# Kernel tuning notes

Hardware: AMD Instinct MI355X
Metric: run time of the kernel (lower is better)

The kernel has to match this reference:

```python
import jax, jax.numpy as jnp
import numpy as np

NHID = 1024
# Canonical DARTS recurrent genotype: (activation, predecessor-state index)
GENOTYPE = [("sigmoid", 0), ("relu", 1), ("relu", 1), ("identity", 1),
            ("tanh", 2), ("sigmoid", 5), ("tanh", 3), ("relu", 5)]
CONCAT = [1, 2, 3, 4, 5, 6, 7, 8]

_ACTS = {"tanh": jnp.tanh, "relu": jax.nn.relu,
         "sigmoid": jax.nn.sigmoid, "identity": lambda z: z}


def _cell(x, h_prev, W0, Ws):
    # x: [B, ninp], h_prev: [B, nhid]
    xh = jnp.concatenate([x, h_prev], axis=-1)              # [B, ninp+nhid]
    c0, h0 = jnp.split(xh @ W0, 2, axis=-1)                 # each [B, nhid]
    s0 = h_prev + jax.nn.sigmoid(c0) * (jnp.tanh(h0) - h_prev)
    states = [s0]
    for i, (name, pred) in enumerate(GENOTYPE):
        s_prev = states[pred]
        c, h = jnp.split(s_prev @ Ws[i], 2, axis=-1)
        s = s_prev + jax.nn.sigmoid(c) * (_ACTS[name](h) - s_prev)
        states.append(s)
    return jnp.mean(jnp.stack([states[i] for i in CONCAT], axis=-1), axis=-1)


def setup_inputs() -> dict:
    key = jax.random.key(0)
    k1, k2, k3 = jax.random.split(key, 3)
    T, B, NINP = 256, 256, 1024
    inputs = jax.random.normal(k1, (T, B, NINP), dtype=jnp.float32)
    h0 = jnp.zeros((B, NHID), dtype=jnp.float32)
    W0 = jax.random.normal(k2, (NINP + NHID, 2 * NHID), dtype=jnp.float32) * 0.02
    Ws = jax.random.normal(k3, (len(GENOTYPE), NHID, 2 * NHID), dtype=jnp.float32) * 0.02
    return {"inputs": inputs, "h0": h0, "W0": W0, "Ws": Ws}


def reference(inputs, h0, W0, Ws):
    def step(h, x):
        h_new = _cell(x, h, W0, Ws)
        return h_new, h_new
    _, hiddens = jax.lax.scan(step, h0, inputs)             # [T, B, nhid]
    return hiddens
```

## Files before the change

### kernel.cpp

```cpp
#include <hip/hip_runtime.h>


typedef short short8 __attribute__((ext_vector_type(8)));
typedef float floatx4 __attribute__((ext_vector_type(4)));

__device__ __forceinline__ unsigned short f2bf(float f) {
  unsigned u = __builtin_bit_cast(unsigned, f);
  u += 0x7fffu + ((u >> 16) & 1u);
  return (unsigned short)(u >> 16);
}

enum { ACT_SIG = 0, ACT_RELU = 1, ACT_TANH = 2, ACT_ID = 3 };

__device__ __forceinline__ float actf(int a, float h) {
  if (a == ACT_SIG)  return 1.f / (1.f + __expf(-h));
  if (a == ACT_RELU) return fmaxf(h, 0.f);
  if (a == ACT_TANH) return 1.f - 2.f / (__expf(2.f * h) + 1.f);
  return h;
}

struct Job {
  const float* A;
  const float* A2;
  const unsigned short* Wt;
  const float* base;
  float* out;
  int act;
  int pad;
};
struct Jobs3 { Job j[3]; };

__global__ __launch_bounds__(256) void cell_gemm(Jobs3 jobs, int K) {
  const Job jb = jobs.j[blockIdx.z];
  const int j0c = blockIdx.x * 32;
  const int m0  = blockIdx.y * 64;

  __shared__ __align__(16) unsigned short As[64][40];
  __shared__ __align__(16) unsigned short Bs[64][40];

  const int tid  = threadIdx.x;
  const int r    = tid >> 2;
  const int kq   = (tid & 3) * 8;
  const int lane = tid & 63;
  const int wave = tid >> 6;
  const int col  = lane & 15;
  const int quad = lane >> 4;

  floatx4 acc[4];
#pragma unroll
  for (int i = 0; i < 4; ++i) acc[i] = (floatx4){0.f, 0.f, 0.f, 0.f};

  const int n_glob = (r < 32) ? (j0c + r) : (1024 + j0c + (r - 32));
  const unsigned short* wrow = jb.Wt + (size_t)n_glob * K;

  for (int k0 = 0; k0 < K; k0 += 32) {
    const float* Ap; int kk;
    if (jb.A2 != nullptr && k0 >= 1024) { Ap = jb.A2; kk = k0 - 1024; }
    else                                { Ap = jb.A;  kk = k0; }

    const float4* ap = reinterpret_cast<const float4*>(Ap + (size_t)(m0 + r) * 1024 + kk + kq);
    float4 f0 = ap[0];
    float4 f1 = ap[1];
    uint4 packed;
    packed.x = (unsigned)f2bf(f0.x) | ((unsigned)f2bf(f0.y) << 16);
    packed.y = (unsigned)f2bf(f0.z) | ((unsigned)f2bf(f0.w) << 16);
    packed.z = (unsigned)f2bf(f1.x) | ((unsigned)f2bf(f1.y) << 16);
    packed.w = (unsigned)f2bf(f1.z) | ((unsigned)f2bf(f1.w) << 16);
    *reinterpret_cast<uint4*>(&As[r][kq]) = packed;

    *reinterpret_cast<uint4*>(&Bs[r][kq]) =
        *reinterpret_cast<const uint4*>(wrow + k0 + kq);

    __syncthreads();

    short8 a = *reinterpret_cast<const short8*>(&As[wave * 16 + col][quad * 8]);
#pragma unroll
    for (int nt = 0; nt < 4; ++nt) {
      short8 b = *reinterpret_cast<const short8*>(&Bs[nt * 16 + col][quad * 8]);
      acc[nt] = __builtin_amdgcn_mfma_f32_16x16x32_bf16(a, b, acc[nt], 0, 0, 0);
    }
    __syncthreads();
  }

#pragma unroll
  for (int nt = 0; nt < 2; ++nt) {
#pragma unroll
    for (int rr = 0; rr < 4; ++rr) {
      int m = m0 + wave * 16 + quad * 4 + rr;
      int n = j0c + nt * 16 + col;
      float c = acc[nt][rr];
      float h = acc[nt + 2][rr];
      float p = jb.base[(size_t)m * 1024 + n];
      float g = 1.f / (1.f + __expf(-c));
      float av = actf(jb.act, h);
      jb.out[(size_t)m * 1024 + n] = fmaf(g, av - p, p);
    }
  }
}

__global__ __launch_bounds__(256) void conv_w(const float* __restrict__ W0,
                                              const float* __restrict__ Wsrc,
                                              unsigned short* __restrict__ wt) {
  int job = blockIdx.z;
  int K = (job == 0) ? 2048 : 1024;
  int kt = blockIdx.y;
  if (kt * 32 >= K) return;
  int nt = blockIdx.x;
  const float* W = (job == 0) ? W0 : (Wsrc + (size_t)(job - 1) * 1024 * 2048);
  unsigned short* Wt = (job == 0) ? wt
      : (wt + (size_t)2048 * 2048 + (size_t)(job - 1) * 2048 * 1024);

  __shared__ unsigned short tile[32][33];
  int tx = threadIdx.x & 31;
  int ty = threadIdx.x >> 5;
#pragma unroll
  for (int i = 0; i < 4; ++i) {
    int k = kt * 32 + ty + i * 8;
    tile[ty + i * 8][tx] = f2bf(W[(size_t)k * 2048 + nt * 32 + tx]);
  }
  __syncthreads();
#pragma unroll
  for (int i = 0; i < 4; ++i) {
    int n = nt * 32 + ty + i * 8;
    Wt[(size_t)n * K + kt * 32 + tx] = tile[tx][ty + i * 8];
  }
}

__global__ __launch_bounds__(256) void mean8(
    const float* __restrict__ s1, const float* __restrict__ s2,
    const float* __restrict__ s3, const float* __restrict__ s4,
    const float* __restrict__ s5, const float* __restrict__ s6,
    const float* __restrict__ s7, const float* __restrict__ s8,
    float* __restrict__ out) {
  int i = blockIdx.x * 256 + threadIdx.x;
  float4 v1 = reinterpret_cast<const float4*>(s1)[i];
  float4 v2 = reinterpret_cast<const float4*>(s2)[i];
  float4 v3 = reinterpret_cast<const float4*>(s3)[i];
  float4 v4 = reinterpret_cast<const float4*>(s4)[i];
  float4 v5 = reinterpret_cast<const float4*>(s5)[i];
  float4 v6 = reinterpret_cast<const float4*>(s6)[i];
  float4 v7 = reinterpret_cast<const float4*>(s7)[i];
  float4 v8 = reinterpret_cast<const float4*>(s8)[i];
  float4 o;
  o.x = (v1.x + v2.x + v3.x + v4.x + v5.x + v6.x + v7.x + v8.x) * 0.125f;
  o.y = (v1.y + v2.y + v3.y + v4.y + v5.y + v6.y + v7.y + v8.y) * 0.125f;
  o.z = (v1.z + v2.z + v3.z + v4.z + v5.z + v6.z + v7.z + v8.z) * 0.125f;
  o.w = (v1.w + v2.w + v3.w + v4.w + v5.w + v6.w + v7.w + v8.w) * 0.125f;
  reinterpret_cast<float4*>(out)[i] = o;
}

extern "C" void kernel_launch(void* const* d_in, const int* in_sizes, int n_in,
                              void* d_out, int out_size, void* d_ws, size_t ws_size,
                              hipStream_t stream) {
  const float* x_all = (const float*)d_in[0];
  const float* h0    = (const float*)d_in[1];
  const float* W0    = (const float*)d_in[2];
  const float* Ws    = (const float*)d_in[3];
  float* out = (float*)d_out;

  unsigned short* wt0 = (unsigned short*)d_ws;
  unsigned short* wts[8];
  for (int i = 0; i < 8; ++i)
    wts[i] = wt0 + (size_t)2048 * 2048 + (size_t)i * 2048 * 1024;
  float* sbuf = (float*)((char*)d_ws + (size_t)(2048 * 2048 + 8 * 2048 * 1024) * 2);
  float* s[9];
  for (int i = 0; i < 9; ++i) s[i] = sbuf + (size_t)i * 256 * 1024;

  conv_w<<<dim3(64, 64, 9), 256, 0, stream>>>(W0, Ws, wt0);

  const size_t BH = (size_t)256 * 1024;
  for (int t = 0; t < 256; ++t) {
    const float* x_t = x_all + (size_t)t * BH;
    const float* hp  = (t == 0) ? h0 : (out + (size_t)(t - 1) * BH);
    float* o_t = out + (size_t)t * BH;

    Jobs3 J{};
    J.j[0] = { x_t, hp, wt0, hp, s[0], ACT_TANH, 0 };
    cell_gemm<<<dim3(32, 4, 1), 256, 0, stream>>>(J, 2048);

    J = Jobs3{};
    J.j[0] = { s[0], nullptr, wts[0], s[0], s[1], ACT_SIG, 0 };
    cell_gemm<<<dim3(32, 4, 1), 256, 0, stream>>>(J, 1024);

    J = Jobs3{};
    J.j[0] = { s[1], nullptr, wts[1], s[1], s[2], ACT_RELU, 0 };
    J.j[1] = { s[1], nullptr, wts[2], s[1], s[3], ACT_RELU, 0 };
    J.j[2] = { s[1], nullptr, wts[3], s[1], s[4], ACT_ID,   0 };
    cell_gemm<<<dim3(32, 4, 3), 256, 0, stream>>>(J, 1024);

    J = Jobs3{};
    J.j[0] = { s[2], nullptr, wts[4], s[2], s[5], ACT_TANH, 0 };
    J.j[1] = { s[3], nullptr, wts[6], s[3], s[7], ACT_TANH, 0 };
    cell_gemm<<<dim3(32, 4, 2), 256, 0, stream>>>(J, 1024);

    J = Jobs3{};
    J.j[0] = { s[5], nullptr, wts[5], s[5], s[6], ACT_SIG,  0 };
    J.j[1] = { s[5], nullptr, wts[7], s[5], s[8], ACT_RELU, 0 };
    cell_gemm<<<dim3(32, 4, 2), 256, 0, stream>>>(J, 1024);

    mean8<<<dim3(256), 256, 0, stream>>>(s[1], s[2], s[3], s[4],
                                         s[5], s[6], s[7], s[8], o_t);
  }
}
```

Measured before the change: 46.12 ms.

## Keep states in bf16, drop LDS staging, fuse final phase with mean and next-input prep

Each stage now writes a bf16 copy of its output, so the next GEMM reads bf16 operands directly instead of converting fp32 activations on every load. The GEMM drops shared-memory tiling for direct register loads with double-buffered MFMA on larger 64x64 per-block tiles. Launches are rebalanced: the identity branch moves to the third phase, and the last two GEMMs, the 8-way mean, and packing of the next x_t/h into a bf16 buffer are fused into one kernel. This removes the separate mean kernel and repeated fp32→bf16 conversion, at the cost of fewer blocks per launch (64 vs 128) and uncoalesced-ish direct global loads with no LDS reuse.

```diff
diff --git a/kernel.cpp b/kernel.cpp
--- a/kernel.cpp
+++ b/kernel.cpp
@@ -3,6 +3,10 @@
 
 typedef short short8 __attribute__((ext_vector_type(8)));
 typedef float floatx4 __attribute__((ext_vector_type(4)));
+
+#define MFMA __builtin_amdgcn_mfma_f32_16x16x32_bf16
+
+enum { ACT_SIG = 0, ACT_RELU = 1, ACT_TANH = 2, ACT_ID = 3 };
 
 __device__ __forceinline__ unsigned short f2bf(float f) {
   unsigned u = __builtin_bit_cast(unsigned, f);
@@ -10,92 +14,209 @@
   return (unsigned short)(u >> 16);
 }
 
-enum { ACT_SIG = 0, ACT_RELU = 1, ACT_TANH = 2, ACT_ID = 3 };
+__device__ __forceinline__ float sigf(float z) { return 1.f / (1.f + __expf(-z)); }
 
 __device__ __forceinline__ float actf(int a, float h) {
-  if (a == ACT_SIG)  return 1.f / (1.f + __expf(-h));
+  if (a == ACT_SIG)  return sigf(h);
   if (a == ACT_RELU) return fmaxf(h, 0.f);
   if (a == ACT_TANH) return 1.f - 2.f / (__expf(2.f * h) + 1.f);
   return h;
 }
 
-struct Job {
-  const float* A;
-  const float* A2;
+
+struct GJob {
+  const unsigned short* A;
   const unsigned short* Wt;
   const float* base;
-  float* out;
+  float* out_f;
+  unsigned short* out_b;
   int act;
-  int pad;
+  int K;
 };
-struct Jobs3 { Job j[3]; };
-
-__global__ __launch_bounds__(256) void cell_gemm(Jobs3 jobs, int K) {
-  const Job jb = jobs.j[blockIdx.z];
-  const int j0c = blockIdx.x * 32;
-  const int m0  = blockIdx.y * 64;
-
-  __shared__ __align__(16) unsigned short As[64][40];
-  __shared__ __align__(16) unsigned short Bs[64][40];
-
-  const int tid  = threadIdx.x;
-  const int r    = tid >> 2;
-  const int kq   = (tid & 3) * 8;
-  const int lane = tid & 63;
-  const int wave = tid >> 6;
-  const int col  = lane & 15;
-  const int quad = lane >> 4;
-
-  floatx4 acc[4];
-#pragma unroll
-  for (int i = 0; i < 4; ++i) acc[i] = (floatx4){0.f, 0.f, 0.f, 0.f};
-
-  const int n_glob = (r < 32) ? (j0c + r) : (1024 + j0c + (r - 32));
-  const unsigned short* wrow = jb.Wt + (size_t)n_glob * K;
-
-  for (int k0 = 0; k0 < K; k0 += 32) {
-    const float* Ap; int kk;
-    if (jb.A2 != nullptr && k0 >= 1024) { Ap = jb.A2; kk = k0 - 1024; }
-    else                                { Ap = jb.A;  kk = k0; }
-
-    const float4* ap = reinterpret_cast<const float4*>(Ap + (size_t)(m0 + r) * 1024 + kk + kq);
-    float4 f0 = ap[0];
-    float4 f1 = ap[1];
-    uint4 packed;
-    packed.x = (unsigned)f2bf(f0.x) | ((unsigned)f2bf(f0.y) << 16);
-    packed.y = (unsigned)f2bf(f0.z) | ((unsigned)f2bf(f0.w) << 16);
-    packed.z = (unsigned)f2bf(f1.x) | ((unsigned)f2bf(f1.y) << 16);
-    packed.w = (unsigned)f2bf(f1.z) | ((unsigned)f2bf(f1.w) << 16);
-    *reinterpret_cast<uint4*>(&As[r][kq]) = packed;
-
-    *reinterpret_cast<uint4*>(&Bs[r][kq]) =
-        *reinterpret_cast<const uint4*>(wrow + k0 + kq);
-
-    __syncthreads();
-
-    short8 a = *reinterpret_cast<const short8*>(&As[wave * 16 + col][quad * 8]);
-#pragma unroll
-    for (int nt = 0; nt < 4; ++nt) {
-      short8 b = *reinterpret_cast<const short8*>(&Bs[nt * 16 + col][quad * 8]);
-      acc[nt] = __builtin_amdgcn_mfma_f32_16x16x32_bf16(a, b, acc[nt], 0, 0, 0);
+struct GJobs { GJob j[3]; };
+
+struct Set6 { short8 a0, a1, b0, b1, b2, b3; };
+
+__device__ __forceinline__ void load6(Set6& s,
+    const unsigned short* pa0, const unsigned short* pa1,
+    const unsigned short* pb0, const unsigned short* pb1,
+    const unsigned short* pb2, const unsigned short* pb3, int k) {
+  s.a0 = *(const short8*)(pa0 + k);
+  s.a1 = *(const short8*)(pa1 + k);
+  s.b0 = *(const short8*)(pb0 + k);
+  s.b1 = *(const short8*)(pb1 + k);
+  s.b2 = *(const short8*)(pb2 + k);
+  s.b3 = *(const short8*)(pb3 + k);
+}
+
+__device__ __forceinline__ void mm6(const Set6& s, floatx4 ac[2][2], floatx4 ah[2][2]) {
+  ac[0][0] = MFMA(s.a0, s.b0, ac[0][0], 0, 0, 0);
+  ac[1][0] = MFMA(s.a1, s.b0, ac[1][0], 0, 0, 0);
+  ac[0][1] = MFMA(s.a0, s.b1, ac[0][1], 0, 0, 0);
+  ac[1][1] = MFMA(s.a1, s.b1, ac[1][1], 0, 0, 0);
+  ah[0][0] = MFMA(s.a0, s.b2, ah[0][0], 0, 0, 0);
+  ah[1][0] = MFMA(s.a1, s.b2, ah[1][0], 0, 0, 0);
+  ah[0][1] = MFMA(s.a0, s.b3, ah[0][1], 0, 0, 0);
+  ah[1][1] = MFMA(s.a1, s.b3, ah[1][1], 0, 0, 0);
+}
+
+__global__ __launch_bounds__(256) void phase_gemm(GJobs jobs) {
+  const GJob jb = jobs.j[blockIdx.z];
+  const int K = jb.K;
+  const int lane = threadIdx.x & 63;
+  const int wave = threadIdx.x >> 6;
+  const int col = lane & 15, quad = lane >> 4;
+  const int m0  = blockIdx.y * 64 + (wave >> 1) * 32;
+  const int sc0 = blockIdx.x * 64 + (wave & 1) * 32;
+
+  const unsigned short* pa0 = jb.A + (size_t)(m0 + col) * K + quad * 8;
+  const unsigned short* pa1 = pa0 + (size_t)16 * K;
+  const unsigned short* pb0 = jb.Wt + (size_t)(sc0 + col) * K + quad * 8;
+  const unsigned short* pb1 = pb0 + (size_t)16 * K;
+  const unsigned short* pb2 = jb.Wt + (size_t)(1024 + sc0 + col) * K + quad * 8;
+  const unsigned short* pb3 = pb2 + (size_t)16 * K;
+
+  floatx4 ac[2][2], ah[2][2];
+#pragma unroll
+  for (int i = 0; i < 2; ++i)
+#pragma unroll
+    for (int j = 0; j < 2; ++j) {
+      ac[i][j] = (floatx4){0.f, 0.f, 0.f, 0.f};
+      ah[i][j] = (floatx4){0.f, 0.f, 0.f, 0.f};
     }
-    __syncthreads();
-  }
-
-#pragma unroll
-  for (int nt = 0; nt < 2; ++nt) {
-#pragma unroll
-    for (int rr = 0; rr < 4; ++rr) {
-      int m = m0 + wave * 16 + quad * 4 + rr;
-      int n = j0c + nt * 16 + col;
-      float c = acc[nt][rr];
-      float h = acc[nt + 2][rr];
-      float p = jb.base[(size_t)m * 1024 + n];
-      float g = 1.f / (1.f + __expf(-c));
-      float av = actf(jb.act, h);
-      jb.out[(size_t)m * 1024 + n] = fmaf(g, av - p, p);
-    }
-  }
+
+  Set6 s0, s1;
+  load6(s0, pa0, pa1, pb0, pb1, pb2, pb3, 0);
+  load6(s1, pa0, pa1, pb0, pb1, pb2, pb3, 32);
+  for (int k = 64; k < K; k += 64) {
+    mm6(s0, ac, ah);
+    load6(s0, pa0, pa1, pb0, pb1, pb2, pb3, k);
+    mm6(s1, ac, ah);
+    load6(s1, pa0, pa1, pb0, pb1, pb2, pb3, k + 32);
+  }
+  mm6(s0, ac, ah);
+  mm6(s1, ac, ah);
+
+  const int act = jb.act;
+#pragma unroll
+  for (int mi = 0; mi < 2; ++mi)
+#pragma unroll
+    for (int ni = 0; ni < 2; ++ni)
+#pragma unroll
+      for (int rr = 0; rr < 4; ++rr) {
+        int m = m0 + mi * 16 + quad * 4 + rr;
+        int n = sc0 + ni * 16 + col;
+        int idx = m * 1024 + n;
+        float c = ac[mi][ni][rr];
+        float h = ah[mi][ni][rr];
+        float p = jb.base[idx];
+        float v = fmaf(sigf(c), actf(act, h) - p, p);
+        jb.out_f[idx] = v;
+        if (jb.out_b) jb.out_b[idx] = f2bf(v);
+      }
+}
+
+struct Set10 { short8 a0, a1, u0, u1, u2, u3, v0, v1, v2, v3; };
+
+__global__ __launch_bounds__(256) void phase_e(
+    const unsigned short* __restrict__ A,
+    const unsigned short* __restrict__ W5t,
+    const unsigned short* __restrict__ W7t,
+    const float* __restrict__ m1, const float* __restrict__ m2,
+    const float* __restrict__ m3, const float* __restrict__ m4,
+    const float* __restrict__ m5, const float* __restrict__ m7,
+    const float* __restrict__ xnext,
+    float* __restrict__ out_t,
+    unsigned short* __restrict__ xhb) {
+  const int lane = threadIdx.x & 63;
+  const int wave = threadIdx.x >> 6;
+  const int col = lane & 15, quad = lane >> 4;
+  const int m0  = blockIdx.y * 64 + (wave >> 1) * 32;
+  const int sc0 = blockIdx.x * 64 + (wave & 1) * 32;
+  const int K = 1024;
+
+  const unsigned short* pa0 = A + (size_t)(m0 + col) * K + quad * 8;
+  const unsigned short* pa1 = pa0 + (size_t)16 * K;
+  const unsigned short* pu0 = W5t + (size_t)(sc0 + col) * K + quad * 8;
+  const unsigned short* pu1 = pu0 + (size_t)16 * K;
+  const unsigned short* pu2 = W5t + (size_t)(1024 + sc0 + col) * K + quad * 8;
+  const unsigned short* pu3 = pu2 + (size_t)16 * K;
+  const unsigned short* pv0 = W7t + (size_t)(sc0 + col) * K + quad * 8;
+  const unsigned short* pv1 = pv0 + (size_t)16 * K;
+  const unsigned short* pv2 = W7t + (size_t)(1024 + sc0 + col) * K + quad * 8;
+  const unsigned short* pv3 = pv2 + (size_t)16 * K;
+
+  floatx4 acc[4][2][2];
+#pragma unroll
+  for (int w = 0; w < 4; ++w)
+#pragma unroll
+    for (int i = 0; i < 2; ++i)
+#pragma unroll
+      for (int j = 0; j < 2; ++j) acc[w][i][j] = (floatx4){0.f, 0.f, 0.f, 0.f};
+
+  Set10 s0, s1;
+#define LOAD10(s, k)                                     \
+  do {                                                   \
+    s.a0 = *(const short8*)(pa0 + (k));                  \
+    s.a1 = *(const short8*)(pa1 + (k));                  \
+    s.u0 = *(const short8*)(pu0 + (k));                  \
+    s.u1 = *(const short8*)(pu1 + (k));                  \
+    s.u2 = *(const short8*)(pu2 + (k));                  \
+    s.u3 = *(const short8*)(pu3 + (k));                  \
+    s.v0 = *(const short8*)(pv0 + (k));                  \
+    s.v1 = *(const short8*)(pv1 + (k));                  \
+    s.v2 = *(const short8*)(pv2 + (k));                  \
+    s.v3 = *(const short8*)(pv3 + (k));                  \
+  } while (0)
+#define MM10(s)                                          \
+  do {                                                   \
+    acc[0][0][0] = MFMA(s.a0, s.u0, acc[0][0][0], 0,0,0);\
+    acc[0][1][0] = MFMA(s.a1, s.u0, acc[0][1][0], 0,0,0);\
+    acc[0][0][1] = MFMA(s.a0, s.u1, acc[0][0][1], 0,0,0);\
+    acc[0][1][1] = MFMA(s.a1, s.u1, acc[0][1][1], 0,0,0);\
+    acc[1][0][0] = MFMA(s.a0, s.u2, acc[1][0][0], 0,0,0);\
+    acc[1][1][0] = MFMA(s.a1, s.u2, acc[1][1][0], 0,0,0);\
+    acc[1][0][1] = MFMA(s.a0, s.u3, acc[1][0][1], 0,0,0);\
+    acc[1][1][1] = MFMA(s.a1, s.u3, acc[1][1][1], 0,0,0);\
+    acc[2][0][0] = MFMA(s.a0, s.v0, acc[2][0][0], 0,0,0);\
+    acc[2][1][0] = MFMA(s.a1, s.v0, acc[2][1][0], 0,0,0);\
+    acc[2][0][1] = MFMA(s.a0, s.v1, acc[2][0][1], 0,0,0);\
+    acc[2][1][1] = MFMA(s.a1, s.v1, acc[2][1][1], 0,0,0);\
+    acc[3][0][0] = MFMA(s.a0, s.v2, acc[3][0][0], 0,0,0);\
+    acc[3][1][0] = MFMA(s.a1, s.v2, acc[3][1][0], 0,0,0);\
+    acc[3][0][1] = MFMA(s.a0, s.v3, acc[3][0][1], 0,0,0);\
+    acc[3][1][1] = MFMA(s.a1, s.v3, acc[3][1][1], 0,0,0);\
+  } while (0)
+
+  LOAD10(s0, 0);
+  LOAD10(s1, 32);
+  for (int k = 64; k < K; k += 64) {
+    MM10(s0);
+    LOAD10(s0, k);
+    MM10(s1);
+    LOAD10(s1, k + 32);
+  }
+  MM10(s0);
+  MM10(s1);
+
+#pragma unroll
+  for (int mi = 0; mi < 2; ++mi)
+#pragma unroll
+    for (int ni = 0; ni < 2; ++ni)
+#pragma unroll
+      for (int rr = 0; rr < 4; ++rr) {
+        int m = m0 + mi * 16 + quad * 4 + rr;
+        int n = sc0 + ni * 16 + col;
+        int idx = m * 1024 + n;
+        float b = m5[idx];
+        float s6 = fmaf(sigf(acc[0][mi][ni][rr]), sigf(acc[1][mi][ni][rr]) - b, b);
+        float s8 = fmaf(sigf(acc[2][mi][ni][rr]), fmaxf(acc[3][mi][ni][rr], 0.f) - b, b);
+        float sum = m1[idx] + m2[idx] + m3[idx] + m4[idx] + b + m7[idx] + s6 + s8;
+        float hh = sum * 0.125f;
+        out_t[idx] = hh;
+        xhb[m * 2048 + 1024 + n] = f2bf(hh);
+        xhb[m * 2048 + n] = f2bf(xnext[idx]);
+      }
 }
 
 __global__ __launch_bounds__(256) void conv_w(const float* __restrict__ W0,
@@ -126,27 +247,13 @@
   }
 }
 
-__global__ __launch_bounds__(256) void mean8(
-    const float* __restrict__ s1, const float* __restrict__ s2,
-    const float* __restrict__ s3, const float* __restrict__ s4,
-    const float* __restrict__ s5, const float* __restrict__ s6,
-    const float* __restrict__ s7, const float* __restrict__ s8,
-    float* __restrict__ out) {
+__global__ __launch_bounds__(256) void init_xh(const float* __restrict__ x0,
+                                               const float* __restrict__ h0,
+                                               unsigned short* __restrict__ xhb) {
   int i = blockIdx.x * 256 + threadIdx.x;
-  float4 v1 = reinterpret_cast<const float4*>(s1)[i];
-  float4 v2 = reinterpret_cast<const float4*>(s2)[i];
-  float4 v3 = reinterpret_cast<const float4*>(s3)[i];
-  float4 v4 = reinterpret_cast<const float4*>(s4)[i];
-  float4 v5 = reinterpret_cast<const float4*>(s5)[i];
-  float4 v6 = reinterpret_cast<const float4*>(s6)[i];
-  float4 v7 = reinterpret_cast<const float4*>(s7)[i];
-  float4 v8 = reinterpret_cast<const float4*>(s8)[i];
-  float4 o;
-  o.x = (v1.x + v2.x + v3.x + v4.x + v5.x + v6.x + v7.x + v8.x) * 0.125f;
-  o.y = (v1.y + v2.y + v3.y + v4.y + v5.y + v6.y + v7.y + v8.y) * 0.125f;
-  o.z = (v1.z + v2.z + v3.z + v4.z + v5.z + v6.z + v7.z + v8.z) * 0.125f;
-  o.w = (v1.w + v2.w + v3.w + v4.w + v5.w + v6.w + v7.w + v8.w) * 0.125f;
-  reinterpret_cast<float4*>(out)[i] = o;
+  int m = i >> 10, n = i & 1023;
+  xhb[m * 2048 + n] = f2bf(x0[i]);
+  xhb[m * 2048 + 1024 + n] = f2bf(h0[i]);
 }
 
 extern "C" void kernel_launch(void* const* d_in, const int* in_sizes, int n_in,
@@ -158,47 +265,51 @@
   const float* Ws    = (const float*)d_in[3];
   float* out = (float*)d_out;
 
+  const size_t BH = (size_t)256 * 1024;
+
   unsigned short* wt0 = (unsigned short*)d_ws;
   unsigned short* wts[8];
   for (int i = 0; i < 8; ++i)
     wts[i] = wt0 + (size_t)2048 * 2048 + (size_t)i * 2048 * 1024;
-  float* sbuf = (float*)((char*)d_ws + (size_t)(2048 * 2048 + 8 * 2048 * 1024) * 2);
-  float* s[9];
-  for (int i = 0; i < 9; ++i) s[i] = sbuf + (size_t)i * 256 * 1024;
+  float* smbase = (float*)((char*)d_ws +
+      (size_t)(2048 * 2048 + 8 * 2048 * 1024) * 2);
+  float* sm[7];
+  for (int i = 0; i < 7; ++i) sm[i] = smbase + (size_t)i * BH;
+  unsigned short* sbbase = (unsigned short*)(smbase + (size_t)7 * BH);
+  unsigned short* sb[5];
+  for (int i = 0; i < 5; ++i) sb[i] = sbbase + (size_t)i * BH;
+  unsigned short* xhb = sbbase + (size_t)5 * BH;
 
   conv_w<<<dim3(64, 64, 9), 256, 0, stream>>>(W0, Ws, wt0);
-
-  const size_t BH = (size_t)256 * 1024;
+  init_xh<<<dim3(1024), 256, 0, stream>>>(x_all, h0, xhb);
+
   for (int t = 0; t < 256; ++t) {
-    const float* x_t = x_all + (size_t)t * BH;
-    const float* hp  = (t == 0) ? h0 : (out + (size_t)(t - 1) * BH);
+    const float* hp = (t == 0) ? h0 : (out + (size_t)(t - 1) * BH);
     float* o_t = out + (size_t)t * BH;
-
-    Jobs3 J{};
-    J.j[0] = { x_t, hp, wt0, hp, s[0], ACT_TANH, 0 };
-    cell_gemm<<<dim3(32, 4, 1), 256, 0, stream>>>(J, 2048);
-
-    J = Jobs3{};
-    J.j[0] = { s[0], nullptr, wts[0], s[0], s[1], ACT_SIG, 0 };
-    cell_gemm<<<dim3(32, 4, 1), 256, 0, stream>>>(J, 1024);
-
-    J = Jobs3{};
-    J.j[0] = { s[1], nullptr, wts[1], s[1], s[2], ACT_RELU, 0 };
-    J.j[1] = { s[1], nullptr, wts[2], s[1], s[3], ACT_RELU, 0 };
-    J.j[2] = { s[1], nullptr, wts[3], s[1], s[4], ACT_ID,   0 };
-    cell_gemm<<<dim3(32, 4, 3), 256, 0, stream>>>(J, 1024);
-
-    J = Jobs3{};
-    J.j[0] = { s[2], nullptr, wts[4], s[2], s[5], ACT_TANH, 0 };
-    J.j[1] = { s[3], nullptr, wts[6], s[3], s[7], ACT_TANH, 0 };
-    cell_gemm<<<dim3(32, 4, 2), 256, 0, stream>>>(J, 1024);
-
-    J = Jobs3{};
-    J.j[0] = { s[5], nullptr, wts[5], s[5], s[6], ACT_SIG,  0 };
-    J.j[1] = { s[5], nullptr, wts[7], s[5], s[8], ACT_RELU, 0 };
-    cell_gemm<<<dim3(32, 4, 2), 256, 0, stream>>>(J, 1024);
-
-    mean8<<<dim3(256), 256, 0, stream>>>(s[1], s[2], s[3], s[4],
-                                         s[5], s[6], s[7], s[8], o_t);
-  }
-}
+    const float* xnext = x_all + (size_t)((t < 255) ? t + 1 : 255) * BH;
+
+    GJobs J{};
+    J.j[0] = { xhb, wt0, hp, sm[0], sb[0], ACT_TANH, 2048 };
+    phase_gemm<<<dim3(16, 4, 1), 256, 0, stream>>>(J);
+
+    J = GJobs{};
+    J.j[0] = { sb[0], wts[0], sm[0], sm[1], sb[1], ACT_SIG, 1024 };
+    phase_gemm<<<dim3(16, 4, 1), 256, 0, stream>>>(J);
+
+    J = GJobs{};
+    J.j[0] = { sb[1], wts[1], sm[1], sm[2], sb[2], ACT_RELU, 1024 };
+    J.j[1] = { sb[1], wts[2], sm[1], sm[3], sb[3], ACT_RELU, 1024 };
+    phase_gemm<<<dim3(16, 4, 2), 256, 0, stream>>>(J);
+
+    J = GJobs{};
+    J.j[0] = { sb[2], wts[4], sm[2], sm[5], sb[4], ACT_TANH, 1024 };
+    J.j[1] = { sb[3], wts[6], sm[3], sm[6], nullptr, ACT_TANH, 1024 };
+    J.j[2] = { sb[1], wts[3], sm[1], sm[4], nullptr, ACT_ID, 1024 };
+    phase_gemm<<<dim3(16, 4, 3), 256, 0, stream>>>(J);
+
+    phase_e<<<dim3(16, 4, 1), 256, 0, stream>>>(
+        sb[4], wts[5], wts[7],
+        sm[1], sm[2], sm[3], sm[4], sm[5], sm[6],
+        xnext, o_t, xhb);
+  }
+}
```

New measurement: 44.55 ms. -3.4%, faster.
